# Kernel tuning notes

Measured on AMD Instinct MI355X. Metric: run time of the kernel, lower is better.

## Reference

```python
import jax, jax.numpy as jnp
import numpy as np

HIDDEN = 4096
N_HEADS = 32
N_KV = 8
HEAD_DIM = 128
ROPE_THETA = 10000.0
B, S = 2, 2048


def _rope_neox(x, cos, sin):
    # x: [B,S,H,D]; cos/sin: [B,S,1,D/2]
    half = x.shape[-1] // 2
    x1, x2 = x[..., :half], x[..., half:]
    return jnp.concatenate([x1 * cos - x2 * sin, x2 * cos + x1 * sin], axis=-1)


def setup_inputs() -> dict:
    key = jax.random.key(0)
    k1, k2, k3 = jax.random.split(key, 3)
    hidden_states = jax.random.normal(k1, (B, S, HIDDEN), dtype=jnp.float32)
    positions = jnp.arange(B * S, dtype=jnp.int32).reshape(B, S)
    q_size = N_HEADS * HEAD_DIM
    kv_size = N_KV * HEAD_DIM
    w_qkv = jax.random.normal(k2, (HIDDEN, q_size + 2 * kv_size), dtype=jnp.float32) * (HIDDEN ** -0.5)
    w_o = jax.random.normal(k3, (q_size, HIDDEN), dtype=jnp.float32) * (q_size ** -0.5)
    return {"hidden_states": hidden_states, "positions": positions, "w_qkv": w_qkv, "w_o": w_o}


def reference(hidden_states, positions, w_qkv, w_o):
    q_size = N_HEADS * HEAD_DIM
    kv_size = N_KV * HEAD_DIM
    b, s, _ = hidden_states.shape

    qkv = hidden_states @ w_qkv  # [B,S,q+2kv]
    q = qkv[..., :q_size].reshape(b, s, N_HEADS, HEAD_DIM)
    k = qkv[..., q_size:q_size + kv_size].reshape(b, s, N_KV, HEAD_DIM)
    v = qkv[..., q_size + kv_size:].reshape(b, s, N_KV, HEAD_DIM)

    # RoPE (neox style, full rotary dim)
    inv_freq = 1.0 / (ROPE_THETA ** (jnp.arange(0, HEAD_DIM, 2, dtype=jnp.float32) / HEAD_DIM))
    ang = positions.astype(jnp.float32)[..., None] * inv_freq  # [B,S,D/2]
    cos = jnp.cos(ang)[:, :, None, :]
    sin = jnp.sin(ang)[:, :, None, :]
    q = _rope_neox(q, cos, sin)
    k = _rope_neox(k, cos, sin)

    # GQA: expand kv heads to match q heads
    rep = N_HEADS // N_KV
    k = jnp.repeat(k, rep, axis=2)  # [B,S,H,D]
    v = jnp.repeat(v, rep, axis=2)

    scale = HEAD_DIM ** -0.5
    scores = jnp.einsum('bqhd,bkhd->bhqk', q, k) * scale  # [B,H,S,S]
    causal = jnp.tril(jnp.ones((s, s), dtype=bool))
    scores = jnp.where(causal[None, None], scores, jnp.finfo(scores.dtype).min)
    probs = jax.nn.softmax(scores, axis=-1)
    attn = jnp.einsum('bhqk,bkhd->bqhd', probs, v).reshape(b, s, q_size)
    return attn @ w_o
```

## Files before the change

kernel.cpp:

```cpp
#include <hip/hip_runtime.h>
#include <hip/hip_bf16.h>
#include <stdint.h>
#include <stddef.h>

typedef unsigned short u16;
typedef __bf16 bf16x8 __attribute__((ext_vector_type(8)));
typedef float f32x4 __attribute__((ext_vector_type(4)));
typedef float f32x16 __attribute__((ext_vector_type(16)));
typedef unsigned u32x2 __attribute__((ext_vector_type(2)));

#define NH 32
#define NKV 8
#define HD 128
#define QKV_N 6144
#define SEQ 2048

__device__ __forceinline__ u16 f2b(float x) {
  union { float f; unsigned u; } v; v.f = x;
  unsigned r = v.u + 0x7FFF + ((v.u >> 16) & 1);
  return (u16)(r >> 16);
}
__device__ __forceinline__ float b2f(u16 b) {
  union { float f; unsigned u; } v; v.u = ((unsigned)b) << 16;
  return v.f;
}
__device__ __forceinline__ void gload16(const void* g, void* l) {
  __builtin_amdgcn_global_load_lds((const __attribute__((address_space(1))) unsigned int*)g,
                                   (__attribute__((address_space(3))) unsigned int*)l, 16, 0, 0);
}
__device__ __forceinline__ unsigned pk(float lo, float hi) {
  union { __bf16 h[2]; unsigned w; } u;
  u.h[0] = (__bf16)lo; u.h[1] = (__bf16)hi;
  return u.w;
}
__device__ __forceinline__ void plswap(unsigned& a, unsigned& b) {
  u32x2 r = __builtin_amdgcn_permlane32_swap(a, b, false, false);
  a = r.x; b = r.y;
}
__device__ __forceinline__ float pl_partner_max(float x) {
  unsigned u = __float_as_uint(x);
  u32x2 r = __builtin_amdgcn_permlane32_swap(u, u, false, false);
  return fmaxf(__uint_as_float(r.x), __uint_as_float(r.y));
}
__device__ __forceinline__ float pl_partner_sum(float x) {
  unsigned u = __float_as_uint(x);
  u32x2 r = __builtin_amdgcn_permlane32_swap(u, u, false, false);
  return __uint_as_float(r.x) + __uint_as_float(r.y);
}

__global__ void cast_f32_bf16(const float* __restrict__ in, u16* __restrict__ out, int n) {
  int i = (blockIdx.x * blockDim.x + threadIdx.x) * 4;
  if (i >= n) return;
  float4 v = *(const float4*)&in[i];
  ushort4 o;
  o.x = f2b(v.x); o.y = f2b(v.y); o.z = f2b(v.z); o.w = f2b(v.w);
  *(ushort4*)&out[i] = o;
}

__global__ void cast_transpose(const float* __restrict__ in, u16* __restrict__ out, int K, int N) {
  __shared__ float t[32][33];
  int n0 = blockIdx.x * 32, k0 = blockIdx.y * 32;
  int tx = threadIdx.x, ty = threadIdx.y;
#pragma unroll
  for (int i = 0; i < 4; ++i)
    t[ty + i * 8][tx] = in[(size_t)(k0 + ty + i * 8) * N + n0 + tx];
  __syncthreads();
#pragma unroll
  for (int i = 0; i < 4; ++i)
    out[(size_t)(n0 + ty + i * 8) * K + k0 + tx] = f2b(t[tx][ty + i * 8]);
}

__device__ __forceinline__ void storeC(float* C, size_t i, float v) { C[i] = v; }
__device__ __forceinline__ void storeC(u16* C, size_t i, float v) { C[i] = f2b(v); }

template <typename OutT>
__global__ __launch_bounds__(512, 2) void gemm256(const u16* __restrict__ A, const u16* __restrict__ Bt,
                                                  OutT* __restrict__ C, int M, int N, int K) {
  __shared__ __align__(16) u16 sA[2 * 256 * 64];
  __shared__ __align__(16) u16 sB[2 * 256 * 64];
  const int nbx = N >> 8;
  const int nwg = (M >> 8) * nbx;
  const int cpx = nwg >> 3;
  const int wg = ((int)blockIdx.x & 7) * cpx + ((int)blockIdx.x >> 3);
  const int row0 = (wg / nbx) << 8, col0 = (wg % nbx) << 8;
  const int tid = threadIdx.x, w = tid >> 6, lane = tid & 63;
  const int wm = w >> 2, wn = w & 3;
  const int lq = lane & 15, lh = lane >> 4, x7 = lq & 7;
  const int o0 = (lh ^ x7) << 3, o1 = ((4 + lh) ^ x7) << 3;
  const int sr7 = (tid >> 3) & 7;
  const int nt = K >> 6;

  auto stage = [&](const u16* __restrict__ src, u16* lbase, int rblk, int half, int t) {
#pragma unroll
    for (int c = 0; c < 2; ++c) {
      const int g = c * 512 + tid;
      const int r = g >> 3, gc = g & 7;
      gload16(src + (size_t)(rblk + half * 128 + r) * K + t * 64 + ((gc ^ sr7) << 3),
              lbase + (half * 1024 + c * 512 + (w << 6)) * 8);
    }
  };

  f32x4 acc[4][4][2] = {};

  stage(A, sA, row0, 0, 0);
  stage(Bt, sB, col0, 0, 0);
  stage(Bt, sB, col0, 1, 0);
  stage(A, sA, row0, 1, 0);
  stage(A, sA + 16384, row0, 0, 1);
  stage(Bt, sB + 16384, col0, 0, 1);
  asm volatile("s_waitcnt vmcnt(6)" ::: "memory");
  __builtin_amdgcn_s_barrier();

  for (int t = 0; t < nt; ++t) {
    const int cur = t & 1;
    u16* curA = sA + cur * 16384;
    u16* curB = sB + cur * 16384;
    u16* nxtA = sA + (cur ^ 1) * 16384;
    u16* nxtB = sB + (cur ^ 1) * 16384;
#pragma unroll
    for (int q = 0; q < 4; ++q) {
      const int ah = q >> 1, bh = q & 1;
      bf16x8 af[4][2], bfr[2][2];
      const u16* pa = curA + (ah * 128 + wm * 64 + lq) * 64;
      const u16* pb = curB + (bh * 128 + wn * 32 + lq) * 64;
#pragma unroll
      for (int mi = 0; mi < 4; ++mi) {
        af[mi][0] = *(const bf16x8*)&pa[mi * 1024 + o0];
        af[mi][1] = *(const bf16x8*)&pa[mi * 1024 + o1];
      }
#pragma unroll
      for (int ni = 0; ni < 2; ++ni) {
        bfr[ni][0] = *(const bf16x8*)&pb[ni * 1024 + o0];
        bfr[ni][1] = *(const bf16x8*)&pb[ni * 1024 + o1];
      }
      if (q == 0 && t + 1 < nt) stage(Bt, nxtB, col0, 1, t + 1);
      if (q == 1 && t + 1 < nt) stage(A, nxtA, row0, 1, t + 1);
      if (q == 2 && t + 2 < nt) stage(A, curA, row0, 0, t + 2);
      if (q == 3 && t + 2 < nt) stage(Bt, curB, col0, 0, t + 2);
      __builtin_amdgcn_s_barrier();
      __builtin_amdgcn_s_setprio(1);
#pragma unroll
      for (int ks = 0; ks < 2; ++ks)
#pragma unroll
        for (int mi = 0; mi < 4; ++mi)
#pragma unroll
          for (int ni = 0; ni < 2; ++ni)
            acc[q][mi][ni] = __builtin_amdgcn_mfma_f32_16x16x32_bf16(af[mi][ks], bfr[ni][ks], acc[q][mi][ni], 0, 0, 0);
      __builtin_amdgcn_s_setprio(0);
      if (q == 1) {
        if (t < nt - 1) asm volatile("s_waitcnt vmcnt(8)" ::: "memory");
        else            asm volatile("s_waitcnt vmcnt(0)" ::: "memory");
      }
      if (q == 3 && t < nt - 1) {
        if (t + 1 < nt - 1) asm volatile("s_waitcnt vmcnt(6)" ::: "memory");
        else                asm volatile("s_waitcnt vmcnt(2)" ::: "memory");
      }
      __builtin_amdgcn_s_barrier();
    }
  }

#pragma unroll
  for (int q = 0; q < 4; ++q) {
    const int ah = q >> 1, bh = q & 1;
#pragma unroll
    for (int mi = 0; mi < 4; ++mi)
#pragma unroll
      for (int ni = 0; ni < 2; ++ni)
#pragma unroll
        for (int j = 0; j < 4; ++j) {
          const int row = row0 + ah * 128 + wm * 64 + mi * 16 + lh * 4 + j;
          const int col = col0 + bh * 128 + wn * 32 + ni * 16 + lq;
          storeC(C, (size_t)row * N + col, acc[q][mi][ni][j]);
        }
  }
}

__global__ void rope_kernel(u16* __restrict__ qkv, const int* __restrict__ pos, float qscale) {
  __shared__ float cs[64], sn[64];
  const int row = blockIdx.x;
  const int tid = threadIdx.x;
  if (tid < 64) {
    float p = (float)pos[row];
    float inv = exp2f(-(float)tid * 0.20762050593046f);
    float a = p * inv;
    cs[tid] = cosf(a);
    sn[tid] = sinf(a);
  }
  __syncthreads();
  const size_t base = (size_t)row * QKV_N;
  for (int i = tid; i < 40 * 64; i += 256) {
    const int h = i >> 6, d = i & 63;
    const size_t o = base + h * 128 + d;
    float x1 = b2f(qkv[o]), x2 = b2f(qkv[o + 64]);
    float c = cs[d], s = sn[d];
    float o1 = x1 * c - x2 * s;
    float o2 = x2 * c + x1 * s;
    if (h < NH) { o1 *= qscale; o2 *= qscale; }
    qkv[o] = f2b(o1);
    qkv[o + 64] = f2b(o2);
  }
}

__global__ void v_transpose(const u16* __restrict__ qkv, u16* __restrict__ vt) {
  __shared__ u16 t[32][33];
  const int b = blockIdx.z >> 3, kvh = blockIdx.z & 7;
  const int s0 = blockIdx.x * 32, d0 = blockIdx.y * 32;
  const int tx = threadIdx.x, ty = threadIdx.y;
#pragma unroll
  for (int i = 0; i < 4; ++i)
    t[ty + i * 8][tx] = qkv[(size_t)(b * SEQ + s0 + ty + i * 8) * QKV_N + 5120 + kvh * 128 + d0 + tx];
  __syncthreads();
#pragma unroll
  for (int i = 0; i < 4; ++i)
    vt[(size_t)((b * NKV + kvh) * HD + d0 + ty + i * 8) * SEQ + s0 + tx] = t[tx][ty + i * 8];
}

__global__ __launch_bounds__(512, 2) void attn_kernel(const u16* __restrict__ qkv, const u16* __restrict__ vt,
                                                      u16* __restrict__ attn) {
  __shared__ __align__(16) u16 sK[2][64 * 128];
  __shared__ __align__(16) u16 sV[2][128 * 64];
  const int b = blockIdx.z, h = blockIdx.y;
  const int qt = (b == 0) ? blockIdx.x : 7 - blockIdx.x;
  const int kvh = h >> 2;
  const int qb = qt * 256;
  const int tid = threadIdx.x, w = tid >> 6, lane = tid & 63;
  const int lq = lane & 31, hi = lane >> 5, x7 = lane & 7;
  const int qw = qb + (w << 5);
  const int qa = qw + lq;
  const int nt = 4 * (qt + 1);

  auto stage = [&](int buf, int kt) {
    const int k0 = kt * 64;
#pragma unroll
    for (int c = 0; c < 2; ++c) {
      const int g = c * 512 + tid;
      const int r = g >> 4, gc = g & 15;
      const int gs = gc ^ (r & 7);
      gload16(qkv + (size_t)(b * SEQ + k0 + r) * QKV_N + 4096 + kvh * 128 + gs * 8,
              &sK[buf][(c * 512 + (w << 6)) * 8]);
    }
#pragma unroll
    for (int c = 0; c < 2; ++c) {
      const int g = c * 512 + tid;
      const int r = g >> 3, gc = g & 7;
      const int gs = gc ^ (r & 7);
      gload16(vt + (size_t)((b * NKV + kvh) * HD + r) * SEQ + k0 + gs * 8,
              &sV[buf][(c * 512 + (w << 6)) * 8]);
    }
  };

  stage(0, 0);
  bf16x8 qf[8];
#pragma unroll
  for (int ks = 0; ks < 8; ++ks)
    qf[ks] = *(const bf16x8*)&qkv[(size_t)(b * SEQ + qw + lq) * QKV_N + h * 128 + ks * 16 + 8 * hi];

  f32x16 o[4] = {};
  float mreg = -1e30f, lreg = 0.f;

  asm volatile("s_waitcnt vmcnt(0)" ::: "memory");
  __builtin_amdgcn_s_barrier();

  for (int kt = 0; kt < nt; ++kt) {
    const int cur = kt & 1;
    const int k0 = kt * 64;
    if (kt + 1 < nt) {
      stage(cur ^ 1, kt + 1);
      asm volatile("s_waitcnt vmcnt(4)" ::: "memory");
    } else {
      asm volatile("s_waitcnt vmcnt(0)" ::: "memory");
    }
    __builtin_amdgcn_s_barrier();

    if (k0 <= qw + 31) {
      const u16* sk = sK[cur];
      f32x16 st0 = {}, st1 = {};
      __builtin_amdgcn_s_setprio(1);
#pragma unroll
      for (int ks = 0; ks < 8; ++ks) {
        const int g = ((2 * ks + hi) ^ x7) * 8;
        bf16x8 kf0 = *(const bf16x8*)&sk[lq * 128 + g];
        bf16x8 kf1 = *(const bf16x8*)&sk[(32 + lq) * 128 + g];
        st0 = __builtin_amdgcn_mfma_f32_32x32x16_bf16(kf0, qf[ks], st0, 0, 0, 0);
        st1 = __builtin_amdgcn_mfma_f32_32x32x16_bf16(kf1, qf[ks], st1, 0, 0, 0);
      }
      __builtin_amdgcn_s_setprio(0);
      if (k0 + 63 > qw) {
#pragma unroll
        for (int r = 0; r < 16; ++r) {
          const int cr = (r & 3) + 8 * (r >> 2) + 4 * hi;
          st0[r] = (k0 + cr <= qa) ? st0[r] : -1e30f;
          st1[r] = (k0 + 32 + cr <= qa) ? st1[r] : -1e30f;
        }
      }
      float a8[8];
#pragma unroll
      for (int r = 0; r < 8; ++r)
        a8[r] = fmaxf(fmaxf(st0[r], st0[r + 8]), fmaxf(st1[r], st1[r + 8]));
#pragma unroll
      for (int s = 4; s; s >>= 1)
#pragma unroll
        for (int r = 0; r < s; ++r) a8[r] = fmaxf(a8[r], a8[r + s]);
      const float pm = pl_partner_max(a8[0]);
      if (!__all(pm <= mreg + 8.f)) {
        const float mn = fmaxf(mreg, pm);
        const float al = exp2f(mreg - mn);
        lreg *= al;
        mreg = mn;
#pragma unroll
        for (int r = 0; r < 16; ++r) {
          const int cr = (r & 3) + 8 * (r >> 2) + 4 * hi;
          const float ar = __shfl(al, cr, 64);
#pragma unroll
          for (int dn = 0; dn < 4; ++dn) o[dn][r] *= ar;
        }
      }
#pragma unroll
      for (int r = 0; r < 16; ++r) {
        st0[r] = exp2f(st0[r] - mreg);
        st1[r] = exp2f(st1[r] - mreg);
      }
      float s8[8];
#pragma unroll
      for (int r = 0; r < 8; ++r)
        s8[r] = (st0[r] + st0[r + 8]) + (st1[r] + st1[r + 8]);
#pragma unroll
      for (int s = 4; s; s >>= 1)
#pragma unroll
        for (int r = 0; r < s; ++r) s8[r] += s8[r + s];
      lreg += pl_partner_sum(s8[0]);
      union U8 { unsigned w[4]; bf16x8 v; };
      U8 pa[4];
#define PACKFRAG(F, P0, P1, P2, P3, P4, P5, P6, P7)                   \
      {                                                               \
        unsigned a0 = pk(P0, P1), a1 = pk(P2, P3);                    \
        unsigned b0 = pk(P4, P5), b1 = pk(P6, P7);                    \
        plswap(a0, b0); plswap(a1, b1);                               \
        pa[F].w[0] = a0; pa[F].w[1] = a1; pa[F].w[2] = b0; pa[F].w[3] = b1; \
      }
      PACKFRAG(0, st0[0], st0[1], st0[2], st0[3], st0[4], st0[5], st0[6], st0[7])
      PACKFRAG(1, st0[8], st0[9], st0[10], st0[11], st0[12], st0[13], st0[14], st0[15])
      PACKFRAG(2, st1[0], st1[1], st1[2], st1[3], st1[4], st1[5], st1[6], st1[7])
      PACKFRAG(3, st1[8], st1[9], st1[10], st1[11], st1[12], st1[13], st1[14], st1[15])
#undef PACKFRAG
      const u16* sv = sV[cur];
      __builtin_amdgcn_s_setprio(1);
#pragma unroll
      for (int dn = 0; dn < 4; ++dn) {
#pragma unroll
        for (int ks = 0; ks < 4; ++ks) {
          bf16x8 vf = *(const bf16x8*)&sv[(dn * 32 + lq) * 64 + (((2 * ks + hi) ^ x7)) * 8];
          o[dn] = __builtin_amdgcn_mfma_f32_32x32x16_bf16(pa[ks].v, vf, o[dn], 0, 0, 0);
        }
      }
      __builtin_amdgcn_s_setprio(0);
    }
    __builtin_amdgcn_s_barrier();
  }

  const float inv = 1.0f / lreg;
#pragma unroll
  for (int r = 0; r < 16; ++r) {
    const int cr = (r & 3) + 8 * (r >> 2) + 4 * hi;
    const float fr = __shfl(inv, cr, 64);
    const size_t row = (size_t)(b * SEQ + qw + cr);
#pragma unroll
    for (int dn = 0; dn < 4; ++dn)
      attn[row * 4096 + h * 128 + dn * 32 + lq] = f2b(o[dn][r] * fr);
  }
}

extern "C" void kernel_launch(void* const* d_in, const int* in_sizes, int n_in,
                              void* d_out, int out_size, void* d_ws, size_t ws_size,
                              hipStream_t stream) {
  const float* hs = (const float*)d_in[0];
  const int* pos = (const int*)d_in[1];
  const float* w_qkv = (const float*)d_in[2];
  const float* w_o = (const float*)d_in[3];
  float* out = (float*)d_out;
  char* ws = (char*)d_ws;

  u16* hid = (u16*)ws;
  u16* attnb = hid;
  u16* wT = (u16*)(ws + 33554432);
  u16* qkv = (u16*)(ws + 83886080);
  u16* vt = (u16*)(ws + 134217728);

  const float qscale = 0.12751744f;

  cast_f32_bf16<<<16384, 256, 0, stream>>>(hs, hid, 4096 * 4096);
  cast_transpose<<<dim3(192, 128), dim3(32, 8), 0, stream>>>(w_qkv, wT, 4096, QKV_N);
  gemm256<u16><<<384, 512, 0, stream>>>(hid, wT, qkv, 4096, QKV_N, 4096);
  rope_kernel<<<4096, 256, 0, stream>>>(qkv, pos, qscale);
  v_transpose<<<dim3(64, 4, 16), dim3(32, 8), 0, stream>>>(qkv, vt);
  cast_transpose<<<dim3(128, 128), dim3(32, 8), 0, stream>>>(w_o, wT, 4096, 4096);
  attn_kernel<<<dim3(8, 32, 2), 512, 0, stream>>>(qkv, vt, attnb);
  gemm256<float><<<256, 512, 0, stream>>>(attnb, wT, out, 4096, 4096, 4096);
}
```

Baseline: 589.5 us.

## Restructure GEMM K-loop into two phases reusing B fragments across A halves

The four quarter-phases per K-tile become two halves. Each half loads one A half-tile and reuses B fragments for both B halves, which are loaded once per tile and kept in registers. This cuts LDS reads of B and halves the barrier count per iteration, since the global prefetch stages are now issued in pairs. In exchange it raises register pressure from the extra B fragments and changes how LDS reads, global loads and MFMA work interleave, with adjusted vmcnt waits.

```diff
diff --git a/kernel.cpp b/kernel.cpp
--- a/kernel.cpp
+++ b/kernel.cpp
@@ -117,46 +117,72 @@
     u16* curB = sB + cur * 16384;
     u16* nxtA = sA + (cur ^ 1) * 16384;
     u16* nxtB = sB + (cur ^ 1) * 16384;
-#pragma unroll
-    for (int q = 0; q < 4; ++q) {
-      const int ah = q >> 1, bh = q & 1;
-      bf16x8 af[4][2], bfr[2][2];
-      const u16* pa = curA + (ah * 128 + wm * 64 + lq) * 64;
-      const u16* pb = curB + (bh * 128 + wn * 32 + lq) * 64;
+
+    bf16x8 af[4][2], bfr[2][2][2];
+    {
+      const u16* pa = curA + (wm * 64 + lq) * 64;
 #pragma unroll
       for (int mi = 0; mi < 4; ++mi) {
         af[mi][0] = *(const bf16x8*)&pa[mi * 1024 + o0];
         af[mi][1] = *(const bf16x8*)&pa[mi * 1024 + o1];
       }
 #pragma unroll
-      for (int ni = 0; ni < 2; ++ni) {
-        bfr[ni][0] = *(const bf16x8*)&pb[ni * 1024 + o0];
-        bfr[ni][1] = *(const bf16x8*)&pb[ni * 1024 + o1];
-      }
-      if (q == 0 && t + 1 < nt) stage(Bt, nxtB, col0, 1, t + 1);
-      if (q == 1 && t + 1 < nt) stage(A, nxtA, row0, 1, t + 1);
-      if (q == 2 && t + 2 < nt) stage(A, curA, row0, 0, t + 2);
-      if (q == 3 && t + 2 < nt) stage(Bt, curB, col0, 0, t + 2);
-      __builtin_amdgcn_s_barrier();
-      __builtin_amdgcn_s_setprio(1);
-#pragma unroll
-      for (int ks = 0; ks < 2; ++ks)
-#pragma unroll
-        for (int mi = 0; mi < 4; ++mi)
-#pragma unroll
-          for (int ni = 0; ni < 2; ++ni)
-            acc[q][mi][ni] = __builtin_amdgcn_mfma_f32_16x16x32_bf16(af[mi][ks], bfr[ni][ks], acc[q][mi][ni], 0, 0, 0);
-      __builtin_amdgcn_s_setprio(0);
-      if (q == 1) {
-        if (t < nt - 1) asm volatile("s_waitcnt vmcnt(8)" ::: "memory");
-        else            asm volatile("s_waitcnt vmcnt(0)" ::: "memory");
-      }
-      if (q == 3 && t < nt - 1) {
-        if (t + 1 < nt - 1) asm volatile("s_waitcnt vmcnt(6)" ::: "memory");
-        else                asm volatile("s_waitcnt vmcnt(2)" ::: "memory");
-      }
-      __builtin_amdgcn_s_barrier();
-    }
+      for (int bh = 0; bh < 2; ++bh) {
+        const u16* pb = curB + (bh * 128 + wn * 32 + lq) * 64;
+#pragma unroll
+        for (int ni = 0; ni < 2; ++ni) {
+          bfr[bh][ni][0] = *(const bf16x8*)&pb[ni * 1024 + o0];
+          bfr[bh][ni][1] = *(const bf16x8*)&pb[ni * 1024 + o1];
+        }
+      }
+    }
+    if (t + 1 < nt) {
+      stage(Bt, nxtB, col0, 1, t + 1);
+      stage(A, nxtA, row0, 1, t + 1);
+    }
+    __builtin_amdgcn_s_barrier();
+    __builtin_amdgcn_s_setprio(1);
+#pragma unroll
+    for (int ks = 0; ks < 2; ++ks)
+#pragma unroll
+      for (int mi = 0; mi < 4; ++mi)
+#pragma unroll
+        for (int ni = 0; ni < 2; ++ni) {
+          acc[0][mi][ni] = __builtin_amdgcn_mfma_f32_16x16x32_bf16(af[mi][ks], bfr[0][ni][ks], acc[0][mi][ni], 0, 0, 0);
+          acc[1][mi][ni] = __builtin_amdgcn_mfma_f32_16x16x32_bf16(af[mi][ks], bfr[1][ni][ks], acc[1][mi][ni], 0, 0, 0);
+        }
+    __builtin_amdgcn_s_setprio(0);
+    if (t < nt - 1) asm volatile("s_waitcnt vmcnt(8)" ::: "memory");
+    else            asm volatile("s_waitcnt vmcnt(0)" ::: "memory");
+    __builtin_amdgcn_s_barrier();
+
+    {
+      const u16* pa = curA + (128 + wm * 64 + lq) * 64;
+#pragma unroll
+      for (int mi = 0; mi < 4; ++mi) {
+        af[mi][0] = *(const bf16x8*)&pa[mi * 1024 + o0];
+        af[mi][1] = *(const bf16x8*)&pa[mi * 1024 + o1];
+      }
+    }
+    if (t + 2 < nt) {
+      stage(A, curA, row0, 0, t + 2);
+      stage(Bt, curB, col0, 0, t + 2);
+    }
+    __builtin_amdgcn_s_barrier();
+    __builtin_amdgcn_s_setprio(1);
+#pragma unroll
+    for (int ks = 0; ks < 2; ++ks)
+#pragma unroll
+      for (int mi = 0; mi < 4; ++mi)
+#pragma unroll
+        for (int ni = 0; ni < 2; ++ni) {
+          acc[2][mi][ni] = __builtin_amdgcn_mfma_f32_16x16x32_bf16(af[mi][ks], bfr[0][ni][ks], acc[2][mi][ni], 0, 0, 0);
+          acc[3][mi][ni] = __builtin_amdgcn_mfma_f32_16x16x32_bf16(af[mi][ks], bfr[1][ni][ks], acc[3][mi][ni], 0, 0, 0);
+        }
+    __builtin_amdgcn_s_setprio(0);
+    if (t < nt - 2)       asm volatile("s_waitcnt vmcnt(6)" ::: "memory");
+    else if (t == nt - 2) asm volatile("s_waitcnt vmcnt(2)" ::: "memory");
+    __builtin_amdgcn_s_barrier();
   }
 
 #pragma unroll
```

After: 538.9 us. -8.6%, faster.
